# Kernel optimization log

Measured on AMD Instinct MI355X. Metric: run time of the kernel, lower is better.

The kernel has to match this reference:

```python
import jax, jax.numpy as jnp
import numpy as np

D = 50          # half-window
K = 2 * D + 1   # 101 window positions
P_SIZE = 100    # predictive-alignment hidden dim


def setup_inputs() -> dict:
    key = jax.random.key(0)
    ks = jax.random.split(key, 5)
    B, S, CQ, CC = 2, 2048, 256, 256
    q = jax.random.normal(ks[0], (B, S, CQ), jnp.float32)
    c_t = jax.random.normal(ks[1], (B, S, CC), jnp.float32)
    W_a = jax.random.normal(ks[2], (CC, CQ), jnp.float32) / np.sqrt(CQ).astype(np.float32)
    W_p = jax.random.normal(ks[3], (P_SIZE, CC), jnp.float32) / np.sqrt(CC).astype(np.float32)
    V_p = jax.random.normal(ks[4], (1, P_SIZE), jnp.float32) / np.sqrt(P_SIZE).astype(np.float32)
    return {"q": q, "c_t": c_t, "W_a": W_a, "W_p": W_p, "V_p": V_p}


def reference(q, c_t, W_a, W_p, V_p):
    B, S, CQ = q.shape
    # predictive alignment: p in (0, S), one predicted center per (b, s)
    p = S * jax.nn.sigmoid(jnp.tanh(c_t @ W_p.T) @ V_p.T)[..., 0]          # [B,S]
    offs = jnp.arange(-D, D + 1)                                           # [K]
    # torch .long() truncates toward zero (raw can be negative)
    raw = jnp.trunc(p[..., None] + offs[None, None, :] + 1.0).astype(jnp.int32)
    # clamp to [0, S+1] then mod (S+1): index 0 == padded (invalid) row,
    # matching torch's NaN-padded row 0 (S+1 wraps to 0 via the modulo)
    idx = jnp.clip(raw, 0, S + 1) % (S + 1)                                # [B,S,K]
    mask = idx == 0                                                        # invalid window slots
    # pad row 0 (torch pads with NaN then zeroes the NaN rows; we pad with 0
    # and mask by index -> identical math for finite q)
    q_pad = jnp.concatenate([jnp.zeros((B, 1, CQ), q.dtype), q], axis=1)   # [B,S+1,CQ]
    gathered = jnp.take_along_axis(q_pad, idx.reshape(B, S * K, 1), axis=1)
    q1 = jnp.where(mask[..., None], 0.0, gathered.reshape(B, S, K, CQ))    # [B,S,K,CQ]
    # score: W_a projection then dot with context
    Wq = jnp.einsum("bskq,cq->bskc", q1, W_a)                              # [B,S,K,CC]
    a = jnp.einsum("bskc,bsc->bsk", Wq, c_t)                               # [B,S,K]
    a = jnp.where(mask, -jnp.inf, a)
    attn = jax.nn.softmax(a, axis=2)                                       # [B,S,K]
    # gaussian decay centered at floor(p) (p > 0 so trunc == floor)
    exponent = -2.0 * (((offs[None, None, :] + jnp.trunc(p)[..., None] - p[..., None]) / D) ** 2)
    w = attn * jnp.exp(exponent)                                           # [B,S,K]
    s_t = jnp.einsum("bsk,bskc->bsc", w, q1)                               # [B,S,CQ]
    return s_t
```

## Files before the change

### kernel.cpp

```cpp
#include <hip/hip_runtime.h>
#include <math.h>

#define S_LEN 2048
#define NB    2
#define CQ_   256
#define CC_   256
#define DH    50
#define KW    101
#define PS    100
#define RB    4
#define HPAD  128

__global__ __launch_bounds__(128) void k_prep(const float* __restrict__ Wp,
                                              float* __restrict__ WpT) {
  const int c = blockIdx.x, j = threadIdx.x;
  WpT[c * HPAD + j] = (j < PS) ? Wp[j * CC_ + c] : 0.0f;
}

__global__ __launch_bounds__(384) void k_align(const float* __restrict__ ct,
    const float* __restrict__ Wa, const float* __restrict__ WpT,
    const float* __restrict__ Vp, float* __restrict__ p_out,
    float* __restrict__ V_out) {
  const int r0  = blockIdx.x * RB;
  const int tid = threadIdx.x;

  __shared__ float sc[RB][CC_];
  {
    const float4* src = (const float4*)(ct + (size_t)r0 * CC_);
    float4* dst = (float4*)&sc[0][0];
    if (tid < RB * CC_ / 4) dst[tid] = src[tid];
  }
  __syncthreads();

  const float* wp;
  int w1s;
  if (tid < CQ_) { wp = Wa + tid;          w1s = CQ_;  }
  else           { wp = WpT + (tid - CQ_); w1s = HPAD; }
  const int w2s = 2 * w1s, w3s = 3 * w1s, w4s = 4 * w1s;

  float acc[RB];
#pragma unroll
  for (int r = 0; r < RB; ++r) acc[r] = 0.0f;

#pragma unroll 2
  for (int c = 0; c < CC_; c += 4) {
    const float w0 = wp[0];
    const float w1 = wp[w1s];
    const float w2 = wp[w2s];
    const float w3 = wp[w3s];
#pragma unroll
    for (int r = 0; r < RB; ++r) {
      const float4 cv = *(const float4*)&sc[r][c];
      float t = acc[r];
      t = fmaf(cv.x, w0, t);
      t = fmaf(cv.y, w1, t);
      t = fmaf(cv.z, w2, t);
      t = fmaf(cv.w, w3, t);
      acc[r] = t;
    }
    wp += w4s;
  }

  if (tid < CQ_) {
#pragma unroll
    for (int r = 0; r < RB; ++r)
      V_out[(size_t)(r0 + r) * CQ_ + tid] = acc[r];
  }

  __shared__ float red[RB][PS + 4];
  if (tid >= CQ_ && tid < CQ_ + PS) {
    const int j = tid - CQ_;
    const float vp = Vp[j];
#pragma unroll
    for (int r = 0; r < RB; ++r) red[r][j] = vp * tanhf(acc[r]);
  }
  __syncthreads();
  if (tid < RB) {
    float s = 0.0f;
    for (int j = 0; j < PS; ++j) s += red[tid][j];
    p_out[r0 + tid] = (float)S_LEN * (1.0f / (1.0f + expf(-s)));
  }
}

__global__ __launch_bounds__(256) void k_attn(const float* __restrict__ q,
    const float* __restrict__ p_in, const float* V,
    float* out) {
  const int wid  = threadIdx.x >> 6;
  const int row  = (blockIdx.x << 2) + wid;
  const int lane = threadIdx.x & 63;
  const int b    = row >> 11;

  __shared__ float ss[4][128];
  __shared__ float sw[4][128];

  const float p  = p_in[row];
  const float tp = truncf(p);
  const float* qb = q + (size_t)b * S_LEN * CQ_;

  const int sub = lane >> 4;
  const int cb  = (lane & 15) * 16;

  const float* vrow = V + (size_t)row * CQ_ + cb;
  const float4 v0 = *(const float4*)(vrow);
  const float4 v1 = *(const float4*)(vrow + 4);
  const float4 v2 = *(const float4*)(vrow + 8);
  const float4 v3 = *(const float4*)(vrow + 12);

  if (lane >= KW - 64) ss[wid][64 + lane] = -INFINITY;

#pragma unroll 2
  for (int g = 0; g < 26; ++g) {
    const int k = (g << 2) + sub;
    const float t = p + (float)(k - DH) + 1.0f;
    const int raw = (int)t;
    const bool ok = (raw >= 1) && (raw <= S_LEN) && (k < KW);
    const int r = ok ? raw - 1 : 0;
    const float* qr = qb + (size_t)r * CQ_ + cb;
    const float4 q0 = *(const float4*)(qr);
    const float4 q1 = *(const float4*)(qr + 4);
    const float4 q2 = *(const float4*)(qr + 8);
    const float4 q3 = *(const float4*)(qr + 12);

    float s = q0.x * v0.x;
    s = fmaf(q0.y, v0.y, s);
    s = fmaf(q0.z, v0.z, s);
    s = fmaf(q0.w, v0.w, s);
    s = fmaf(q1.x, v1.x, s);
    s = fmaf(q1.y, v1.y, s);
    s = fmaf(q1.z, v1.z, s);
    s = fmaf(q1.w, v1.w, s);
    s = fmaf(q2.x, v2.x, s);
    s = fmaf(q2.y, v2.y, s);
    s = fmaf(q2.z, v2.z, s);
    s = fmaf(q2.w, v2.w, s);
    s = fmaf(q3.x, v3.x, s);
    s = fmaf(q3.y, v3.y, s);
    s = fmaf(q3.z, v3.z, s);
    s = fmaf(q3.w, v3.w, s);

    s += __shfl_xor(s, 1, 64);
    s += __shfl_xor(s, 2, 64);
    s += __shfl_xor(s, 4, 64);
    s += __shfl_xor(s, 8, 64);
    s = ok ? s : -INFINITY;
    if ((lane & 15) == 0) ss[wid][k] = s;
  }

  const float s0 = ss[wid][lane];
  const float s1 = ss[wid][64 + lane];

  float m = fmaxf(s0, s1);
#pragma unroll
  for (int off = 1; off < 64; off <<= 1) m = fmaxf(m, __shfl_xor(m, off, 64));

  const float e0 = __expf(s0 - m);
  const float e1 = __expf(s1 - m);
  float den = e0 + e1;
#pragma unroll
  for (int off = 1; off < 64; off <<= 1) den += __shfl_xor(den, off, 64);
  const float inv = 1.0f / den;

  float g0 = ((float)(lane - DH) + tp - p) / (float)DH;
  float g1 = ((float)(lane + (64 - DH)) + tp - p) / (float)DH;
  const float w0 = e0 * __expf(-2.0f * g0 * g0) * inv;
  const float w1 = e1 * __expf(-2.0f * g1 * g1) * inv;
  sw[wid][lane] = w0;
  if (lane < KW - 64) sw[wid][64 + lane] = w1;

  float4 acc = make_float4(0.0f, 0.0f, 0.0f, 0.0f);
  for (int k = 0; k < KW; ++k) {
    const float wk = sw[wid][k];
    if (wk > 1e-5f) {
      const float t = p + (float)(k - DH) + 1.0f;
      const int r   = (int)t - 1;
      const float4 qv = *(const float4*)(qb + (size_t)r * CQ_ + lane * 4);
      acc.x = fmaf(wk, qv.x, acc.x);
      acc.y = fmaf(wk, qv.y, acc.y);
      acc.z = fmaf(wk, qv.z, acc.z);
      acc.w = fmaf(wk, qv.w, acc.w);
    }
  }
  *(float4*)(out + (size_t)row * CQ_ + lane * 4) = acc;
}

extern "C" void kernel_launch(void* const* d_in, const int* in_sizes, int n_in,
                              void* d_out, int out_size, void* d_ws, size_t ws_size,
                              hipStream_t stream) {
  const float* q  = (const float*)d_in[0];
  const float* ct = (const float*)d_in[1];
  const float* Wa = (const float*)d_in[2];
  const float* Wp = (const float*)d_in[3];
  const float* Vp = (const float*)d_in[4];
  float* out = (float*)d_out;

  float* ws     = (float*)d_ws;
  float* p_ws   = ws;
  float* WpT_ws = ws + NB * S_LEN;

  k_prep <<<CC_, HPAD, 0, stream>>>(Wp, WpT_ws);
  k_align<<<(NB * S_LEN) / RB, 384, 0, stream>>>(ct, Wa, WpT_ws, Vp, p_ws, out);
  k_attn <<<(NB * S_LEN) / 4, 256, 0, stream>>>(q, p_ws, out, out);
}
```

Baseline: 128.1 us.

## Restructure alignment projection with more rows per block and ballot-driven weighted sum

k_align now handles 8 rows per block using 256 threads. Half the threads compute two W_a columns each using float2 loads, and the other half compute the W_p hidden units. Context rows are read straight from global memory instead of being staged in shared memory. In k_attn, the shared weight array and its serial scan over all 101 slots are replaced by wave ballots over the threshold, which iterate only over the active slots and broadcast each weight with a shuffle. The score dot product is split into four independent accumulators and unrolled further to add instruction-level parallelism. This changes the floating-point summation order.

```diff
diff --git a/kernel.cpp b/kernel.cpp
--- a/kernel.cpp
+++ b/kernel.cpp
@@ -8,8 +8,9 @@
 #define DH    50
 #define KW    101
 #define PS    100
-#define RB    4
+#define RB    8
 #define HPAD  128
+#define WTH   1e-5f
 
 __global__ __launch_bounds__(128) void k_prep(const float* __restrict__ Wp,
                                               float* __restrict__ WpT) {
@@ -17,62 +18,73 @@
   WpT[c * HPAD + j] = (j < PS) ? Wp[j * CC_ + c] : 0.0f;
 }
 
-__global__ __launch_bounds__(384) void k_align(const float* __restrict__ ct,
+__global__ __launch_bounds__(256) void k_align(const float* __restrict__ ct,
     const float* __restrict__ Wa, const float* __restrict__ WpT,
     const float* __restrict__ Vp, float* __restrict__ p_out,
     float* __restrict__ V_out) {
   const int r0  = blockIdx.x * RB;
   const int tid = threadIdx.x;
-
-  __shared__ float sc[RB][CC_];
-  {
-    const float4* src = (const float4*)(ct + (size_t)r0 * CC_);
-    float4* dst = (float4*)&sc[0][0];
-    if (tid < RB * CC_ / 4) dst[tid] = src[tid];
-  }
-  __syncthreads();
-
-  const float* wp;
-  int w1s;
-  if (tid < CQ_) { wp = Wa + tid;          w1s = CQ_;  }
-  else           { wp = WpT + (tid - CQ_); w1s = HPAD; }
-  const int w2s = 2 * w1s, w3s = 3 * w1s, w4s = 4 * w1s;
-
-  float acc[RB];
-#pragma unroll
-  for (int r = 0; r < RB; ++r) acc[r] = 0.0f;
+  const float* crow = ct + (size_t)r0 * CC_;
+
+  __shared__ float red[RB][PS + 4];
+
+  if (tid < 128) {
+    const float* wa = Wa + 2 * tid;
+    float a0[RB], a1[RB];
+#pragma unroll
+    for (int r = 0; r < RB; ++r) { a0[r] = 0.0f; a1[r] = 0.0f; }
 
 #pragma unroll 2
-  for (int c = 0; c < CC_; c += 4) {
-    const float w0 = wp[0];
-    const float w1 = wp[w1s];
-    const float w2 = wp[w2s];
-    const float w3 = wp[w3s];
+    for (int c = 0; c < CC_; c += 4) {
+      const float2 w0 = *(const float2*)(wa + (size_t)(c + 0) * CQ_);
+      const float2 w1 = *(const float2*)(wa + (size_t)(c + 1) * CQ_);
+      const float2 w2 = *(const float2*)(wa + (size_t)(c + 2) * CQ_);
+      const float2 w3 = *(const float2*)(wa + (size_t)(c + 3) * CQ_);
+#pragma unroll
+      for (int r = 0; r < RB; ++r) {
+        const float4 cv = *(const float4*)&crow[r * CC_ + c];
+        float t0 = a0[r], t1 = a1[r];
+        t0 = fmaf(cv.x, w0.x, t0);  t1 = fmaf(cv.x, w0.y, t1);
+        t0 = fmaf(cv.y, w1.x, t0);  t1 = fmaf(cv.y, w1.y, t1);
+        t0 = fmaf(cv.z, w2.x, t0);  t1 = fmaf(cv.z, w2.y, t1);
+        t0 = fmaf(cv.w, w3.x, t0);  t1 = fmaf(cv.w, w3.y, t1);
+        a0[r] = t0; a1[r] = t1;
+      }
+    }
 #pragma unroll
     for (int r = 0; r < RB; ++r) {
-      const float4 cv = *(const float4*)&sc[r][c];
-      float t = acc[r];
-      t = fmaf(cv.x, w0, t);
-      t = fmaf(cv.y, w1, t);
-      t = fmaf(cv.z, w2, t);
-      t = fmaf(cv.w, w3, t);
-      acc[r] = t;
-    }
-    wp += w4s;
-  }
-
-  if (tid < CQ_) {
-#pragma unroll
-    for (int r = 0; r < RB; ++r)
-      V_out[(size_t)(r0 + r) * CQ_ + tid] = acc[r];
-  }
-
-  __shared__ float red[RB][PS + 4];
-  if (tid >= CQ_ && tid < CQ_ + PS) {
-    const int j = tid - CQ_;
-    const float vp = Vp[j];
-#pragma unroll
-    for (int r = 0; r < RB; ++r) red[r][j] = vp * tanhf(acc[r]);
+      float2 o; o.x = a0[r]; o.y = a1[r];
+      *(float2*)(V_out + (size_t)(r0 + r) * CQ_ + 2 * tid) = o;
+    }
+  } else {
+    const int j = tid - 128;
+    const float* wh = WpT + j;
+    float ah[RB];
+#pragma unroll
+    for (int r = 0; r < RB; ++r) ah[r] = 0.0f;
+
+#pragma unroll 2
+    for (int c = 0; c < CC_; c += 4) {
+      const float w0 = wh[(size_t)(c + 0) * HPAD];
+      const float w1 = wh[(size_t)(c + 1) * HPAD];
+      const float w2 = wh[(size_t)(c + 2) * HPAD];
+      const float w3 = wh[(size_t)(c + 3) * HPAD];
+#pragma unroll
+      for (int r = 0; r < RB; ++r) {
+        const float4 cv = *(const float4*)&crow[r * CC_ + c];
+        float t = ah[r];
+        t = fmaf(cv.x, w0, t);
+        t = fmaf(cv.y, w1, t);
+        t = fmaf(cv.z, w2, t);
+        t = fmaf(cv.w, w3, t);
+        ah[r] = t;
+      }
+    }
+    if (j < PS) {
+      const float vp = Vp[j];
+#pragma unroll
+      for (int r = 0; r < RB; ++r) red[r][j] = vp * tanhf(ah[r]);
+    }
   }
   __syncthreads();
   if (tid < RB) {
@@ -91,7 +103,6 @@
   const int b    = row >> 11;
 
   __shared__ float ss[4][128];
-  __shared__ float sw[4][128];
 
   const float p  = p_in[row];
   const float tp = truncf(p);
@@ -108,7 +119,7 @@
 
   if (lane >= KW - 64) ss[wid][64 + lane] = -INFINITY;
 
-#pragma unroll 2
+#pragma unroll 4
   for (int g = 0; g < 26; ++g) {
     const int k = (g << 2) + sub;
     const float t = p + (float)(k - DH) + 1.0f;
@@ -121,22 +132,23 @@
     const float4 q2 = *(const float4*)(qr + 8);
     const float4 q3 = *(const float4*)(qr + 12);
 
-    float s = q0.x * v0.x;
-    s = fmaf(q0.y, v0.y, s);
-    s = fmaf(q0.z, v0.z, s);
-    s = fmaf(q0.w, v0.w, s);
-    s = fmaf(q1.x, v1.x, s);
-    s = fmaf(q1.y, v1.y, s);
-    s = fmaf(q1.z, v1.z, s);
-    s = fmaf(q1.w, v1.w, s);
-    s = fmaf(q2.x, v2.x, s);
-    s = fmaf(q2.y, v2.y, s);
-    s = fmaf(q2.z, v2.z, s);
-    s = fmaf(q2.w, v2.w, s);
-    s = fmaf(q3.x, v3.x, s);
-    s = fmaf(q3.y, v3.y, s);
-    s = fmaf(q3.z, v3.z, s);
-    s = fmaf(q3.w, v3.w, s);
+    float t0 = q0.x * v0.x;
+    float t1 = q1.x * v1.x;
+    float t2 = q2.x * v2.x;
+    float t3 = q3.x * v3.x;
+    t0 = fmaf(q0.y, v0.y, t0);
+    t1 = fmaf(q1.y, v1.y, t1);
+    t2 = fmaf(q2.y, v2.y, t2);
+    t3 = fmaf(q3.y, v3.y, t3);
+    t0 = fmaf(q0.z, v0.z, t0);
+    t1 = fmaf(q1.z, v1.z, t1);
+    t2 = fmaf(q2.z, v2.z, t2);
+    t3 = fmaf(q3.z, v3.z, t3);
+    t0 = fmaf(q0.w, v0.w, t0);
+    t1 = fmaf(q1.w, v1.w, t1);
+    t2 = fmaf(q2.w, v2.w, t2);
+    t3 = fmaf(q3.w, v3.w, t3);
+    float s = (t0 + t1) + (t2 + t3);
 
     s += __shfl_xor(s, 1, 64);
     s += __shfl_xor(s, 2, 64);
@@ -164,21 +176,34 @@
   float g1 = ((float)(lane + (64 - DH)) + tp - p) / (float)DH;
   const float w0 = e0 * __expf(-2.0f * g0 * g0) * inv;
   const float w1 = e1 * __expf(-2.0f * g1 * g1) * inv;
-  sw[wid][lane] = w0;
-  if (lane < KW - 64) sw[wid][64 + lane] = w1;
+
+  unsigned long long m0 = __ballot(w0 > WTH);
+  unsigned long long m1 = __ballot((lane < KW - 64) && (w1 > WTH));
 
   float4 acc = make_float4(0.0f, 0.0f, 0.0f, 0.0f);
-  for (int k = 0; k < KW; ++k) {
-    const float wk = sw[wid][k];
-    if (wk > 1e-5f) {
-      const float t = p + (float)(k - DH) + 1.0f;
-      const int r   = (int)t - 1;
-      const float4 qv = *(const float4*)(qb + (size_t)r * CQ_ + lane * 4);
-      acc.x = fmaf(wk, qv.x, acc.x);
-      acc.y = fmaf(wk, qv.y, acc.y);
-      acc.z = fmaf(wk, qv.z, acc.z);
-      acc.w = fmaf(wk, qv.w, acc.w);
-    }
+  while (m0) {
+    const int k = __builtin_ctzll(m0);
+    m0 &= m0 - 1;
+    const float wk = __shfl(w0, k, 64);
+    const float t = p + (float)(k - DH) + 1.0f;
+    const int r = (int)t - 1;
+    const float4 qv = *(const float4*)(qb + (size_t)r * CQ_ + lane * 4);
+    acc.x = fmaf(wk, qv.x, acc.x);
+    acc.y = fmaf(wk, qv.y, acc.y);
+    acc.z = fmaf(wk, qv.z, acc.z);
+    acc.w = fmaf(wk, qv.w, acc.w);
+  }
+  while (m1) {
+    const int k = __builtin_ctzll(m1);
+    m1 &= m1 - 1;
+    const float wk = __shfl(w1, k, 64);
+    const float t = p + (float)(k + (64 - DH)) + 1.0f;
+    const int r = (int)t - 1;
+    const float4 qv = *(const float4*)(qb + (size_t)r * CQ_ + lane * 4);
+    acc.x = fmaf(wk, qv.x, acc.x);
+    acc.y = fmaf(wk, qv.y, acc.y);
+    acc.z = fmaf(wk, qv.z, acc.z);
+    acc.w = fmaf(wk, qv.w, acc.w);
   }
   *(float4*)(out + (size_t)row * CQ_ + lane * 4) = acc;
 }
@@ -198,6 +223,6 @@
   float* WpT_ws = ws + NB * S_LEN;
 
   k_prep <<<CC_, HPAD, 0, stream>>>(Wp, WpT_ws);
-  k_align<<<(NB * S_LEN) / RB, 384, 0, stream>>>(ct, Wa, WpT_ws, Vp, p_ws, out);
+  k_align<<<(NB * S_LEN) / RB, 256, 0, stream>>>(ct, Wa, WpT_ws, Vp, p_ws, out);
   k_attn <<<(NB * S_LEN) / 4, 256, 0, stream>>>(q, p_ws, out, out);
 }
```

New measurement: 121.7 us. 1.05x faster.
